# Kernel optimization log

Measured on AMD Instinct MI355X. Metric: run time of the kernel, lower is better.

## Reference

```python
import jax, jax.numpy as jnp
import numpy as np

IN_DIM, OUT_DIM, GRID_N, K = 256, 256, 5, 3
SIZE = IN_DIM * OUT_DIM
BATCH = 256
NB = GRID_N + K  # number of order-K B-spline basis functions


def b_batch(x, grid, k):
    """Cox-de Boor B-spline basis, iterative form of the recursive torch B_batch.
    x: [S, B], grid: [S, G+1] -> returns [S, G+k, B]."""
    h = (grid[:, -1:] - grid[:, :1]) / (grid.shape[1] - 1)
    left = grid[:, :1] - h * jnp.arange(k, 0, -1, dtype=grid.dtype)
    right = grid[:, -1:] + h * jnp.arange(1, k + 1, dtype=grid.dtype)
    g = jnp.concatenate([left, grid, right], axis=1)[:, :, None]  # [S, G+1+2k, 1]
    xb = x[:, None, :]                                            # [S, 1, B]
    B = ((xb >= g[:, :-1]) & (xb < g[:, 1:])).astype(x.dtype)     # order 0
    for j in range(1, k + 1):
        B = ((xb - g[:, :-(j + 1)]) / (g[:, j:-1] - g[:, :-(j + 1)])) * B[:, :-1] \
          + ((g[:, j + 1:] - xb) / (g[:, j + 1:] - g[:, 1:-j])) * B[:, 1:]
    return B


def setup_inputs() -> dict:
    key = jax.random.key(0)
    k1, k2 = jax.random.split(key)
    x = jax.random.normal(k1, (BATCH, IN_DIM), dtype=jnp.float32)
    # grid: same linspace over [-1, 1] replicated for every (in,out) pair
    grid = jnp.tile(jnp.linspace(-1.0, 1.0, GRID_N + 1, dtype=jnp.float32)[None, :], (SIZE, 1))
    coef = 0.1 * jax.random.normal(k2, (SIZE, NB), dtype=jnp.float32)
    scale_base = jnp.ones((SIZE,), dtype=jnp.float32)
    scale_spline = jnp.ones((SIZE,), dtype=jnp.float32)
    return {"x": x, "grid": grid, "coef": coef,
            "scale_base": scale_base, "scale_spline": scale_spline}


def reference(x, grid, coef, scale_base, scale_spline):
    batch = x.shape[0]
    # i[o*in_dim + j, b] = x[b, j]  (torch einsum+reshape+permute)
    i = jnp.tile(x.T, (OUT_DIM, 1))                       # [S, B]
    B = b_batch(i, grid, K)                               # [S, NB, B]
    c = jnp.einsum('sn,snb->bs', coef, B)                 # [B, S]
    base = jax.nn.silu(i).T                               # [B, S]
    a = scale_base[None, :] * base + scale_spline[None, :] * c
    y = a.reshape(batch, OUT_DIM, IN_DIM).sum(axis=2)     # [B, out_dim]
    return y
```

## Files before the change

kernel.cpp:

```cpp
#include <hip/hip_runtime.h>
#include <hip/hip_bf16.h>


#define KK 2304
#define RS 2312
#define SMEM_BYTES (2*16*RS*2)

typedef __attribute__((ext_vector_type(8))) short bf16x8;
typedef __attribute__((ext_vector_type(4))) float f32x4;

__device__ __forceinline__ unsigned short bfbits(float f) {
    __hip_bfloat16 h = __float2bfloat16(f);
    return *reinterpret_cast<unsigned short*>(&h);
}

__global__ __launch_bounds__(1024, 4) void kan_fused(
        const float* __restrict__ x, const float* __restrict__ grid,
        const float* __restrict__ coef, const float* __restrict__ sb,
        const float* __restrict__ ss, float* __restrict__ out) {
    extern __shared__ char smem[];
    __hip_bfloat16* ldsF = (__hip_bfloat16*)smem;
    __hip_bfloat16* ldsW = (__hip_bfloat16*)(smem + 16*RS*2);
    unsigned* ldsWu = (unsigned*)ldsW;

    int tr  = blockIdx.x & 15;
    int tc  = blockIdx.x >> 4;
    int tid = threadIdx.x;

#pragma unroll
    for (int p = 0; p < 5; ++p) {
        int off = tid * 16 + p * 16384;
        if (off < 16 * RS * 2) *(uint4*)((char*)ldsF + off) = uint4{0, 0, 0, 0};
    }

    float gl = grid[0], gr = grid[5];
    float h  = (gr - gl) * 0.2f;
    float g0 = gl - 3.f * h;
    float inv_h = 1.f / h;
    __syncthreads();

#pragma unroll
    for (int it = 0; it < 2; ++it) {
        int pidx = tid + it * 1024;
        int row  = pidx >> 7;
        int dp   = pidx & 127;
        int d0   = dp * 2;

        float2 xv2 = *(const float2*)(x + (tr * 16 + row) * 256 + d0);
        unsigned short sl[2];
        const float k6 = 1.f / 6.f;
#pragma unroll
        for (int e = 0; e < 2; ++e) {
            float xv = (e == 0) ? xv2.x : xv2.y;
            float tt = (xv - g0) * inv_h;
            float fi = floorf(tt);
            int   i  = (int)fi;
            float u  = tt - fi;
            float u2 = u * u, u3 = u2 * u, um = 1.f - u;
            float b3 = u3 * k6;
            float b2 = (-3.f*u3 + 3.f*u2 + 3.f*u + 1.f) * k6;
            float b1 = (3.f*u3 - 6.f*u2 + 4.f) * k6;
            float b0 = um * um * um * k6;
            __hip_bfloat16* base = ldsF + row * RS + d0 + e;
            float vals[4] = {b3, b2, b1, b0};
#pragma unroll
            for (int m = 0; m < 4; ++m) {
                int n = i - m;
                if ((unsigned)n <= 7u)
                    base[n * 256] = __float2bfloat16(vals[m]);
            }
            sl[e] = bfbits(xv / (1.f + __expf(-xv)));
        }
        ldsF[row * RS + 8 * 256 + d0]     = *reinterpret_cast<__hip_bfloat16*>(&sl[0]);
        ldsF[row * RS + 8 * 256 + d0 + 1] = *reinterpret_cast<__hip_bfloat16*>(&sl[1]);

        int s0 = (tc * 16 + row) * 256 + d0;
        float4 a0 = *(const float4*)(coef + (size_t)s0 * 8);
        float4 a1 = *(const float4*)(coef + (size_t)s0 * 8 + 4);
        float4 c0 = *(const float4*)(coef + (size_t)s0 * 8 + 8);
        float4 c1 = *(const float4*)(coef + (size_t)s0 * 8 + 12);
        float2 vb = *(const float2*)(sb + s0);
        float2 vs = *(const float2*)(ss + s0);
        float wa[9] = {vs.x*a0.x, vs.x*a0.y, vs.x*a0.z, vs.x*a0.w,
                       vs.x*a1.x, vs.x*a1.y, vs.x*a1.z, vs.x*a1.w, vb.x};
        float wb[9] = {vs.y*c0.x, vs.y*c0.y, vs.y*c0.z, vs.y*c0.w,
                       vs.y*c1.x, vs.y*c1.y, vs.y*c1.z, vs.y*c1.w, vb.y};
        unsigned ubase = (unsigned)(row * RS + d0) >> 1;
#pragma unroll
        for (int n = 0; n < 9; ++n)
            ldsWu[ubase + n * 128] =
                (unsigned)bfbits(wa[n]) | ((unsigned)bfbits(wb[n]) << 16);
    }
    __syncthreads();

    int lane = tid & 63, wave = tid >> 6;
    int r16 = lane & 15, kg = lane >> 4;
    const __hip_bfloat16* ap = ldsF + r16 * RS + kg * 8;
    const __hip_bfloat16* bp = ldsW + r16 * RS + kg * 8;
    f32x4 acc = {0.f, 0.f, 0.f, 0.f};
    for (int s = wave; s < 72; s += 16) {
        bf16x8 a = *reinterpret_cast<const bf16x8*>(ap + s * 32);
        bf16x8 b = *reinterpret_cast<const bf16x8*>(bp + s * 32);
        acc = __builtin_amdgcn_mfma_f32_16x16x32_bf16(a, b, acc, 0, 0, 0);
    }

    __syncthreads();
    float (*red)[64][4] = (float(*)[64][4])smem;
    *(f32x4*)red[wave][lane] = acc;
    __syncthreads();
    if (tid < 256) {
        int l2 = tid >> 2, j2 = tid & 3;
        float v = 0.f;
#pragma unroll
        for (int w = 0; w < 16; ++w) v += red[w][l2][j2];
        out[(size_t)(tr * 16 + (l2 >> 4) * 4 + j2) * 256 + tc * 16 + (l2 & 15)] = v;
    }
}

extern "C" void kernel_launch(void* const* d_in, const int* in_sizes, int n_in,
                              void* d_out, int out_size, void* d_ws, size_t ws_size,
                              hipStream_t stream) {
    const float* x    = (const float*)d_in[0];
    const float* grid = (const float*)d_in[1];
    const float* coef = (const float*)d_in[2];
    const float* sb   = (const float*)d_in[3];
    const float* ss   = (const float*)d_in[4];
    float* out = (float*)d_out;

    kan_fused<<<256, 1024, SMEM_BYTES, stream>>>(x, grid, coef, sb, ss, out);
}
```

Measured before the change: 10.53 us.

## Hoist global loads before LDS zeroing, remap blocks, pack LDS writes, coalesce output

Moves all global loads of x, coef and the scales ahead of the first barrier, so their latency overlaps with the LDS zero-fill and the grid setup. Remaps block indices so neighbouring blocks share tiles differently, which may change L2 reuse. The LDS zero-fill now clears only the feature region row by row instead of a flat range. The two silu values are written as one packed 32-bit store, and the final reduction is reindexed so output stores are coalesced along columns. The cost is higher register pressure from holding the prefetched values across the barrier.

```diff
diff --git a/kernel.cpp b/kernel.cpp
--- a/kernel.cpp
+++ b/kernel.cpp
@@ -21,22 +21,41 @@
     extern __shared__ char smem[];
     __hip_bfloat16* ldsF = (__hip_bfloat16*)smem;
     __hip_bfloat16* ldsW = (__hip_bfloat16*)(smem + 16*RS*2);
+    unsigned* ldsFu = (unsigned*)ldsF;
     unsigned* ldsWu = (unsigned*)ldsW;
 
-    int tr  = blockIdx.x & 15;
-    int tc  = blockIdx.x >> 4;
+    int blk = blockIdx.x;
+    int tc  = 2 * (blk & 7) + ((blk >> 7) & 1);
+    int tr  = (blk >> 3) & 15;
     int tid = threadIdx.x;
 
 #pragma unroll
-    for (int p = 0; p < 5; ++p) {
-        int off = tid * 16 + p * 16384;
-        if (off < 16 * RS * 2) *(uint4*)((char*)ldsF + off) = uint4{0, 0, 0, 0};
+    for (int p = 0; p < 4; ++p) {
+        int slot = tid + p * 1024;
+        int row  = slot >> 8, c = slot & 255;
+        *(uint4*)(smem + row * (RS * 2) + c * 16) = uint4{0, 0, 0, 0};
     }
 
     float gl = grid[0], gr = grid[5];
     float h  = (gr - gl) * 0.2f;
     float g0 = gl - 3.f * h;
     float inv_h = 1.f / h;
+
+    float2 xv2[2], vb2[2], vs2[2];
+    float4 cf0[2], cf1[2], cf2[2], cf3[2];
+#pragma unroll
+    for (int it = 0; it < 2; ++it) {
+        int pidx = tid + it * 1024;
+        int row  = pidx >> 7;
+        int dp   = pidx & 127;
+        int d0   = dp * 2;
+        xv2[it] = *(const float2*)(x + (tr * 16 + row) * 256 + d0);
+        int s0 = (tc * 16 + row) * 256 + d0;
+        const float4* cp = (const float4*)(coef + (size_t)s0 * 8);
+        cf0[it] = cp[0]; cf1[it] = cp[1]; cf2[it] = cp[2]; cf3[it] = cp[3];
+        vb2[it] = *(const float2*)(sb + s0);
+        vs2[it] = *(const float2*)(ss + s0);
+    }
     __syncthreads();
 
 #pragma unroll
@@ -46,12 +65,12 @@
         int dp   = pidx & 127;
         int d0   = dp * 2;
 
-        float2 xv2 = *(const float2*)(x + (tr * 16 + row) * 256 + d0);
         unsigned short sl[2];
         const float k6 = 1.f / 6.f;
+        float xs[2] = {xv2[it].x, xv2[it].y};
 #pragma unroll
         for (int e = 0; e < 2; ++e) {
-            float xv = (e == 0) ? xv2.x : xv2.y;
+            float xv = xs[e];
             float tt = (xv - g0) * inv_h;
             float fi = floorf(tt);
             int   i  = (int)fi;
@@ -71,21 +90,17 @@
             }
             sl[e] = bfbits(xv / (1.f + __expf(-xv)));
         }
-        ldsF[row * RS + 8 * 256 + d0]     = *reinterpret_cast<__hip_bfloat16*>(&sl[0]);
-        ldsF[row * RS + 8 * 256 + d0 + 1] = *reinterpret_cast<__hip_bfloat16*>(&sl[1]);
+        ldsFu[row * (RS / 2) + 1024 + dp] =
+            (unsigned)sl[0] | ((unsigned)sl[1] << 16);
 
-        int s0 = (tc * 16 + row) * 256 + d0;
-        float4 a0 = *(const float4*)(coef + (size_t)s0 * 8);
-        float4 a1 = *(const float4*)(coef + (size_t)s0 * 8 + 4);
-        float4 c0 = *(const float4*)(coef + (size_t)s0 * 8 + 8);
-        float4 c1 = *(const float4*)(coef + (size_t)s0 * 8 + 12);
-        float2 vb = *(const float2*)(sb + s0);
-        float2 vs = *(const float2*)(ss + s0);
-        float wa[9] = {vs.x*a0.x, vs.x*a0.y, vs.x*a0.z, vs.x*a0.w,
-                       vs.x*a1.x, vs.x*a1.y, vs.x*a1.z, vs.x*a1.w, vb.x};
-        float wb[9] = {vs.y*c0.x, vs.y*c0.y, vs.y*c0.z, vs.y*c0.w,
-                       vs.y*c1.x, vs.y*c1.y, vs.y*c1.z, vs.y*c1.w, vb.y};
-        unsigned ubase = (unsigned)(row * RS + d0) >> 1;
+        float vsx = vs2[it].x, vsy = vs2[it].y;
+        float wa[9] = {vsx*cf0[it].x, vsx*cf0[it].y, vsx*cf0[it].z, vsx*cf0[it].w,
+                       vsx*cf1[it].x, vsx*cf1[it].y, vsx*cf1[it].z, vsx*cf1[it].w,
+                       vb2[it].x};
+        float wb[9] = {vsy*cf2[it].x, vsy*cf2[it].y, vsy*cf2[it].z, vsy*cf2[it].w,
+                       vsy*cf3[it].x, vsy*cf3[it].y, vsy*cf3[it].z, vsy*cf3[it].w,
+                       vb2[it].y};
+        unsigned ubase = (unsigned)(row * (RS / 2) + dp);
 #pragma unroll
         for (int n = 0; n < 9; ++n)
             ldsWu[ubase + n * 128] =
@@ -109,11 +124,12 @@
     *(f32x4*)red[wave][lane] = acc;
     __syncthreads();
     if (tid < 256) {
-        int l2 = tid >> 2, j2 = tid & 3;
+        int row = tid >> 4, col = tid & 15;
+        int l2 = (row >> 2) * 16 + col, j2 = row & 3;
         float v = 0.f;
 #pragma unroll
         for (int w = 0; w < 16; ++w) v += red[w][l2][j2];
-        out[(size_t)(tr * 16 + (l2 >> 4) * 4 + j2) * 256 + tc * 16 + (l2 & 15)] = v;
+        out[(size_t)(tr * 16 + row) * 256 + tc * 16 + col] = v;
     }
 }
 
```

After: 11.51 us. +9.4%, slower.
